# Kernel tuning notes

Hardware: AMD Instinct MI355X
Metric: run time of the kernel (lower is better)

## Reference

```python
import jax, jax.numpy as jnp
import numpy as np

B, D, L, E, R = 16384, 2048, 3, 8, 64


def setup_inputs() -> dict:
    key = jax.random.key(0)
    k1, k2, k3, k4 = jax.random.split(key, 4)
    scale = 1.0 / np.sqrt(D)  # ~ PyTorch Linear default init scale
    X0 = jax.random.normal(k1, (B, D), dtype=jnp.float32)
    U = jax.random.normal(k2, (L, E, R, D), dtype=jnp.float32) * scale
    V = jax.random.normal(k3, (L, E, R, D), dtype=jnp.float32) * scale
    Wg = jax.random.normal(k4, (L, E, D), dtype=jnp.float32) * scale
    bg = jnp.zeros((L, E), dtype=jnp.float32)
    return {"X0": X0, "U": U, "V": V, "Wg": Wg, "bg": bg}


def reference(X0, U, V, Wg, bg):
    # X0: (B, D); U, V: (L, E, R, D); Wg: (L, E, D); bg: (L, E)
    Xi = X0
    num_layers = U.shape[0]
    for l in range(num_layers):  # small fixed layer count
        gate = jax.nn.softmax(jnp.einsum('bd,ed->be', Xi, Wg[l]) + bg[l], axis=1)  # (B, E)
        Uo = jnp.einsum('bd,erd->ber', Xi, U[l])  # (B, E, R)
        Vo = jnp.einsum('bd,erd->ber', Xi, V[l])  # (B, E, R)
        expert_out = jnp.sum(Uo * Vo, axis=2)     # (B, E) low-rank bilinear forms
        xw = jnp.sum(expert_out * gate, axis=1, keepdims=True)  # (B, 1)
        Xi = Xi + X0 * xw  # residual cross update (dropout=0, eval mode)
    return Xi
```

## Files before the change

### kernel.cpp

```cpp
#include <hip/hip_runtime.h>
#include <hip/hip_bf16.h>

#define BDIM 16384
#define DDIM 2048
#define LNUM 3
#define ENUM 8
#define NP 24

#define BM 256
#define BK 64
#define NKIT (DDIM / BK)

typedef _Float16 f16x8 __attribute__((ext_vector_type(8)));
typedef _Float16 f16x4 __attribute__((ext_vector_type(4)));
typedef float f32x16 __attribute__((ext_vector_type(16)));


__global__ void cvt_w_kernel(const float* __restrict__ U, const float* __restrict__ V,
                             _Float16* __restrict__ Whf) {
    int idx = blockIdx.x * 256 + threadIdx.x;
    int f8     = idx & 255;
    int row128 = (idx >> 8) & 127;
    int p      = idx >> 15;
    const float* src = (row128 < 64)
        ? (U + ((size_t)(p * 64 + row128) * DDIM + f8 * 8))
        : (V + ((size_t)(p * 64 + (row128 - 64)) * DDIM + f8 * 8));
    float4 a = ((const float4*)src)[0];
    float4 b = ((const float4*)src)[1];
    f16x8 h = { (_Float16)a.x, (_Float16)a.y, (_Float16)a.z, (_Float16)a.w,
                (_Float16)b.x, (_Float16)b.y, (_Float16)b.z, (_Float16)b.w };
    int gn = row128 >> 5, col = row128 & 31;
    int kw = f8 >> 1, khalf = f8 & 1;
    size_t C = ((size_t)((p * 4 + gn) * 128 + kw)) * 64 + khalf * 32 + col;
    ((f16x8*)Whf)[C] = h;
}

__global__ __launch_bounds__(256, 2) void gate_kernel(
    const float* __restrict__ X0, const float* __restrict__ Wg,
    float* __restrict__ G, _Float16* __restrict__ X0f) {
    __shared__ float Wgs[NP * 256];
    const int tid = (int)threadIdx.x;
    const int rq  = tid >> 3;
    const int q   = tid & 7;
    const int r0  = blockIdx.x * 32 + rq;
    const int g32 = blockIdx.x;

    float acc[NP];
#pragma unroll
    for (int j = 0; j < NP; ++j) acc[j] = 0.f;

    const float4* xp = (const float4*)(X0 + (size_t)r0 * DDIM);

    for (int k0 = 0; k0 < DDIM; k0 += 256) {
        __syncthreads();
#pragma unroll
        for (int t = tid; t < NP * 64; t += 256)
            ((float4*)Wgs)[t] =
                ((const float4*)Wg)[(size_t)(t >> 6) * (DDIM / 4) + (k0 >> 2) + (t & 63)];
        __syncthreads();
#pragma unroll 2
        for (int i = 0; i < 4; ++i) {
            int f8 = i * 8 + q;
            int gcf4 = (k0 >> 2) + f8 * 2;
            float4 xa = xp[gcf4];
            float4 xb = xp[gcf4 + 1];
            f16x8 h = { (_Float16)xa.x, (_Float16)xa.y, (_Float16)xa.z, (_Float16)xa.w,
                        (_Float16)xb.x, (_Float16)xb.y, (_Float16)xb.z, (_Float16)xb.w };
            int kw = (k0 >> 4) + (f8 >> 1);
            int khalf = f8 & 1;
            ((f16x8*)X0f)[((size_t)(g32 * 128 + kw)) * 64 + khalf * 32 + rq] = h;
#pragma unroll
            for (int j = 0; j < NP; ++j) {
                float4 wa = ((const float4*)(Wgs + j * 256))[f8 * 2];
                float4 wb = ((const float4*)(Wgs + j * 256))[f8 * 2 + 1];
                acc[j] += xa.x * wa.x + xa.y * wa.y + xa.z * wa.z + xa.w * wa.w
                        + xb.x * wb.x + xb.y * wb.y + xb.z * wb.z + xb.w * wb.w;
            }
        }
    }
#pragma unroll
    for (int j = 0; j < NP; ++j) {
        float v = acc[j];
        v += __shfl_xor(v, 1);
        v += __shfl_xor(v, 2);
        v += __shfl_xor(v, 4);
        if (q == 0) G[(size_t)j * BDIM + r0] = v;
    }
}

__global__ __launch_bounds__(256, 2) void gemm_t_kernel(
    const _Float16* __restrict__ X0f,
    const _Float16* __restrict__ Whf,
    float* __restrict__ T)
{
    const int p    = blockIdx.y;
    const int m0   = blockIdx.x * BM;
    const int tid  = (int)threadIdx.x;
    const int wave = tid >> 6;
    const int lane = tid & 63;

    __shared__ _Float16 Bs[2 * 16 * 512];

    const int g32b = (m0 >> 5) + wave * 2;

    f32x16 acc[2][4];
#pragma unroll
    for (int i = 0; i < 2; ++i)
#pragma unroll
        for (int j = 0; j < 4; ++j) acc[i][j] = (f32x16)(0.f);

    f16x8 aF[2][8];

#pragma unroll
    for (int kw = 0; kw < 4; ++kw) {
        const _Float16* gb = Whf + (((size_t)((p * 4 + wave) * 128 + kw)) * 64 + lane) * 8;
        __builtin_amdgcn_global_load_lds(
            (const __attribute__((address_space(1))) void*)gb,
            (__attribute__((address_space(3))) void*)&Bs[(wave * 4 + kw) * 512], 16, 0, 0);
    }
#pragma unroll
    for (int mt = 0; mt < 2; ++mt)
#pragma unroll
        for (int kw = 0; kw < 4; ++kw)
            aF[0][mt * 4 + kw] = *(const f16x8*)(
                X0f + (((size_t)((g32b + mt) * 128 + kw)) * 64 + lane) * 8);
    __syncthreads();

#pragma unroll 2
    for (int it = 0; it < NKIT; ++it) {
        const int cur = it & 1, nxt = cur ^ 1;
        if (it != NKIT - 1) {
            const int kwn = (it + 1) * 4;
#pragma unroll
            for (int kw = 0; kw < 4; ++kw) {
                const _Float16* gb =
                    Whf + (((size_t)((p * 4 + wave) * 128 + kwn + kw)) * 64 + lane) * 8;
                __builtin_amdgcn_global_load_lds(
                    (const __attribute__((address_space(1))) void*)gb,
                    (__attribute__((address_space(3))) void*)&Bs[(nxt * 16 + wave * 4 + kw) * 512],
                    16, 0, 0);
            }
#pragma unroll
            for (int mt = 0; mt < 2; ++mt)
#pragma unroll
                for (int kw = 0; kw < 4; ++kw)
                    aF[nxt][mt * 4 + kw] = *(const f16x8*)(
                        X0f + (((size_t)((g32b + mt) * 128 + kwn + kw)) * 64 + lane) * 8);
        }
#pragma unroll
        for (int kw = 0; kw < 4; ++kw) {
            f16x8 bF[4];
#pragma unroll
            for (int gn = 0; gn < 4; ++gn)
                bF[gn] = *(const f16x8*)&Bs[((cur * 16 + gn * 4 + kw) * 64 + lane) * 8];
#pragma unroll
            for (int mt = 0; mt < 2; ++mt)
#pragma unroll
                for (int gn = 0; gn < 4; ++gn)
                    acc[mt][gn] = __builtin_amdgcn_mfma_f32_32x32x16_f16(
                        aF[cur][mt * 4 + kw], bF[gn], acc[mt][gn], 0, 0, 0);
        }
        __syncthreads();
    }

#pragma unroll
    for (int mt = 0; mt < 2; ++mt) {
#pragma unroll
        for (int reg = 0; reg < 16; ++reg) {
            float tp = acc[mt][0][reg] * acc[mt][2][reg]
                     + acc[mt][1][reg] * acc[mt][3][reg];
            tp += __shfl_xor(tp, 1);
            tp += __shfl_xor(tp, 2);
            tp += __shfl_xor(tp, 4);
            tp += __shfl_xor(tp, 8);
            tp += __shfl_xor(tp, 16);
            if ((lane & 31) == 0) {
                int row = (reg & 3) + 8 * (reg >> 2) + 4 * (lane >> 5);
                T[(size_t)p * BDIM + m0 + wave * 64 + mt * 32 + row] = tp;
            }
        }
    }
}

__global__ void epilogue_kernel(const _Float16* __restrict__ X0f,
                                const float* __restrict__ T,
                                const float* __restrict__ G,
                                const float* __restrict__ bg,
                                float* __restrict__ out) {
    __shared__ float s_sh[16];
    const int b0 = blockIdx.x * 16;
    const int tid = (int)threadIdx.x;
    if (tid < 16) {
        int b = b0 + tid;
        float s = 1.f;
#pragma unroll
        for (int l = 0; l < LNUM; ++l) {
            float logit[ENUM];
            float mx = -1e30f;
#pragma unroll
            for (int e = 0; e < ENUM; ++e) {
                int j = l * ENUM + e;
                float g = s * G[(size_t)j * BDIM + b] + bg[j];
                logit[e] = g;
                mx = fmaxf(mx, g);
            }
            float den = 0.f, num = 0.f;
            float s2 = s * s;
#pragma unroll
            for (int e = 0; e < ENUM; ++e) {
                int j = l * ENUM + e;
                float w = __expf(logit[e] - mx);
                den += w;
                num += w * (s2 * T[(size_t)j * BDIM + b]);
            }
            s += num / den;
        }
        s_sh[tid] = s;
    }
    __syncthreads();
    for (int idx = tid; idx < 16 * 256; idx += 256) {
        int r = idx >> 8;
        int c = idx & 255;
        int rg = b0 + r;
        float s = s_sh[r];
        f16x8 h = ((const f16x8*)X0f)[((size_t)((rg >> 5) * 128 + (c >> 1))) * 64
                                      + (c & 1) * 32 + (rg & 31)];
        float4 o0 = { s * (float)h[0], s * (float)h[1], s * (float)h[2], s * (float)h[3] };
        float4 o1 = { s * (float)h[4], s * (float)h[5], s * (float)h[6], s * (float)h[7] };
        float4* op = (float4*)(out + (size_t)rg * DDIM + c * 8);
        op[0] = o0;
        op[1] = o1;
    }
}

extern "C" void kernel_launch(void* const* d_in, const int* in_sizes, int n_in,
                              void* d_out, int out_size, void* d_ws, size_t ws_size,
                              hipStream_t stream) {
    const float* X0 = (const float*)d_in[0];
    const float* U  = (const float*)d_in[1];
    const float* V  = (const float*)d_in[2];
    const float* Wg = (const float*)d_in[3];
    const float* bg = (const float*)d_in[4];
    float* out = (float*)d_out;

    char* ws = (char*)d_ws;
    _Float16* X0f = (_Float16*)ws;
    _Float16* Whf = (_Float16*)(ws + 67108864ull);
    float* T      = (float*)(ws + 67108864ull + 12582912ull);
    float* G      = (float*)(ws + 67108864ull + 12582912ull + 1572864ull);

    cvt_w_kernel<<<dim3(NP * 128 * 256 / 256), dim3(256), 0, stream>>>(U, V, Whf);
    gate_kernel<<<dim3(BDIM / 32), dim3(256), 0, stream>>>(X0, Wg, G, X0f);
    gemm_t_kernel<<<dim3(BDIM / BM, NP), dim3(256), 0, stream>>>(X0f, Whf, T);
    epilogue_kernel<<<dim3(BDIM / 16), dim3(256), 0, stream>>>(X0f, T, G, bg, out);
}
```

Measured before the change: 549.7 us.

## Fuse weight conversion into gate kernel and epilogue into GEMM via counters

Merges the weight fp16 conversion into the gate kernel as extra blocks, and has gate blocks process two 32-row groups each. The GEMM doubles its K step per iteration and reorganises A-fragment prefetching. The last block to finish each 32-row group (tracked with atomic counters) computes the scalar recurrence and writes the output from fp32 X0. This removes two launches and the separate epilogue pass. It adds a memset and atomics, plus a tail where finishing blocks carry the epilogue, and the larger LDS buffer may reduce occupancy.

```diff
diff --git a/kernel.cpp b/kernel.cpp
--- a/kernel.cpp
+++ b/kernel.cpp
@@ -7,49 +7,51 @@
 #define ENUM 8
 #define NP 24
 
-#define BM 256
-#define BK 64
-#define NKIT (DDIM / BK)
+#define NKIT 16
 
 typedef _Float16 f16x8 __attribute__((ext_vector_type(8)));
 typedef _Float16 f16x4 __attribute__((ext_vector_type(4)));
 typedef float f32x16 __attribute__((ext_vector_type(16)));
 
 
-__global__ void cvt_w_kernel(const float* __restrict__ U, const float* __restrict__ V,
-                             _Float16* __restrict__ Whf) {
-    int idx = blockIdx.x * 256 + threadIdx.x;
-    int f8     = idx & 255;
-    int row128 = (idx >> 8) & 127;
-    int p      = idx >> 15;
-    const float* src = (row128 < 64)
-        ? (U + ((size_t)(p * 64 + row128) * DDIM + f8 * 8))
-        : (V + ((size_t)(p * 64 + (row128 - 64)) * DDIM + f8 * 8));
-    float4 a = ((const float4*)src)[0];
-    float4 b = ((const float4*)src)[1];
-    f16x8 h = { (_Float16)a.x, (_Float16)a.y, (_Float16)a.z, (_Float16)a.w,
-                (_Float16)b.x, (_Float16)b.y, (_Float16)b.z, (_Float16)b.w };
-    int gn = row128 >> 5, col = row128 & 31;
-    int kw = f8 >> 1, khalf = f8 & 1;
-    size_t C = ((size_t)((p * 4 + gn) * 128 + kw)) * 64 + khalf * 32 + col;
-    ((f16x8*)Whf)[C] = h;
-}
-
-__global__ __launch_bounds__(256, 2) void gate_kernel(
-    const float* __restrict__ X0, const float* __restrict__ Wg,
-    float* __restrict__ G, _Float16* __restrict__ X0f) {
+#define GATE_BLOCKS 256
+__global__ __launch_bounds__(256, 4) void prep_kernel(
+    const float* __restrict__ X0, const float* __restrict__ U,
+    const float* __restrict__ V, const float* __restrict__ Wg,
+    float* __restrict__ G, _Float16* __restrict__ X0f, _Float16* __restrict__ Whf) {
+    const int tid = (int)threadIdx.x;
+    if (blockIdx.x >= GATE_BLOCKS) {
+        int cidx = (blockIdx.x - GATE_BLOCKS) * 256 + tid;
+        int col   = cidx & 31;
+        int khalf = (cidx >> 5) & 1;
+        int kw    = (cidx >> 6) & 127;
+        int gn    = (cidx >> 13) & 3;
+        int p     = cidx >> 15;
+        int row128 = gn * 32 + col;
+        const float* src = (row128 < 64)
+            ? (U + ((size_t)(p * 64 + row128) * DDIM + kw * 16 + khalf * 8))
+            : (V + ((size_t)(p * 64 + (row128 - 64)) * DDIM + kw * 16 + khalf * 8));
+        float4 a = ((const float4*)src)[0];
+        float4 b = ((const float4*)src)[1];
+        f16x8 h = { (_Float16)a.x, (_Float16)a.y, (_Float16)a.z, (_Float16)a.w,
+                    (_Float16)b.x, (_Float16)b.y, (_Float16)b.z, (_Float16)b.w };
+        ((f16x8*)Whf)[cidx] = h;
+        return;
+    }
     __shared__ float Wgs[NP * 256];
-    const int tid = (int)threadIdx.x;
-    const int rq  = tid >> 3;
-    const int q   = tid & 7;
-    const int r0  = blockIdx.x * 32 + rq;
-    const int g32 = blockIdx.x;
-
-    float acc[NP];
-#pragma unroll
-    for (int j = 0; j < NP; ++j) acc[j] = 0.f;
-
-    const float4* xp = (const float4*)(X0 + (size_t)r0 * DDIM);
+    const int rq = tid >> 3;
+    const int q  = tid & 7;
+    const int r0 = blockIdx.x * 64 + rq;
+    const int g32a = blockIdx.x * 2, g32b_ = g32a + 1;
+
+    float acc[2][NP];
+#pragma unroll
+    for (int r = 0; r < 2; ++r)
+#pragma unroll
+        for (int j = 0; j < NP; ++j) acc[r][j] = 0.f;
+
+    const float4* x0p = (const float4*)(X0 + (size_t)r0 * DDIM);
+    const float4* x1p = (const float4*)(X0 + (size_t)(r0 + 32) * DDIM);
 
     for (int k0 = 0; k0 < DDIM; k0 += 256) {
         __syncthreads();
@@ -60,48 +62,66 @@
         __syncthreads();
 #pragma unroll 2
         for (int i = 0; i < 4; ++i) {
-            int f8 = i * 8 + q;
-            int gcf4 = (k0 >> 2) + f8 * 2;
-            float4 xa = xp[gcf4];
-            float4 xb = xp[gcf4 + 1];
-            f16x8 h = { (_Float16)xa.x, (_Float16)xa.y, (_Float16)xa.z, (_Float16)xa.w,
-                        (_Float16)xb.x, (_Float16)xb.y, (_Float16)xb.z, (_Float16)xb.w };
-            int kw = (k0 >> 4) + (f8 >> 1);
-            int khalf = f8 & 1;
-            ((f16x8*)X0f)[((size_t)(g32 * 128 + kw)) * 64 + khalf * 32 + rq] = h;
+            int f8l = i * 8 + q;
+            int gf4 = (k0 >> 2) + f8l * 2;
+            float4 xa = x0p[gf4], xb = x0p[gf4 + 1];
+            float4 ya = x1p[gf4], yb = x1p[gf4 + 1];
+            int f8g = (k0 >> 3) + f8l;
+            int kw = f8g >> 1, khalf = f8g & 1;
+            f16x8 h0 = { (_Float16)xa.x, (_Float16)xa.y, (_Float16)xa.z, (_Float16)xa.w,
+                         (_Float16)xb.x, (_Float16)xb.y, (_Float16)xb.z, (_Float16)xb.w };
+            f16x8 h1 = { (_Float16)ya.x, (_Float16)ya.y, (_Float16)ya.z, (_Float16)ya.w,
+                         (_Float16)yb.x, (_Float16)yb.y, (_Float16)yb.z, (_Float16)yb.w };
+            ((f16x8*)X0f)[((size_t)(g32a * 128 + kw)) * 64 + khalf * 32 + rq] = h0;
+            ((f16x8*)X0f)[((size_t)(g32b_ * 128 + kw)) * 64 + khalf * 32 + rq] = h1;
 #pragma unroll
             for (int j = 0; j < NP; ++j) {
-                float4 wa = ((const float4*)(Wgs + j * 256))[f8 * 2];
-                float4 wb = ((const float4*)(Wgs + j * 256))[f8 * 2 + 1];
-                acc[j] += xa.x * wa.x + xa.y * wa.y + xa.z * wa.z + xa.w * wa.w
-                        + xb.x * wb.x + xb.y * wb.y + xb.z * wb.z + xb.w * wb.w;
+                float4 wa = ((const float4*)(Wgs + j * 256))[f8l * 2];
+                float4 wb = ((const float4*)(Wgs + j * 256))[f8l * 2 + 1];
+                acc[0][j] += xa.x * wa.x + xa.y * wa.y + xa.z * wa.z + xa.w * wa.w
+                           + xb.x * wb.x + xb.y * wb.y + xb.z * wb.z + xb.w * wb.w;
+                acc[1][j] += ya.x * wa.x + ya.y * wa.y + ya.z * wa.z + ya.w * wa.w
+                           + yb.x * wb.x + yb.y * wb.y + yb.z * wb.z + yb.w * wb.w;
             }
         }
     }
 #pragma unroll
-    for (int j = 0; j < NP; ++j) {
-        float v = acc[j];
-        v += __shfl_xor(v, 1);
-        v += __shfl_xor(v, 2);
-        v += __shfl_xor(v, 4);
-        if (q == 0) G[(size_t)j * BDIM + r0] = v;
-    }
+    for (int r = 0; r < 2; ++r)
+#pragma unroll
+        for (int j = 0; j < NP; ++j) {
+            float v = acc[r][j];
+            v += __shfl_xor(v, 1);
+            v += __shfl_xor(v, 2);
+            v += __shfl_xor(v, 4);
+            if (q == 0) G[(size_t)j * BDIM + r0 + r * 32] = v;
+        }
 }
 
-__global__ __launch_bounds__(256, 2) void gemm_t_kernel(
+__global__ __launch_bounds__(256, 2) void gemm_epi_kernel(
     const _Float16* __restrict__ X0f,
     const _Float16* __restrict__ Whf,
-    float* __restrict__ T)
+    const float* __restrict__ X0,
+    const float* __restrict__ G,
+    const float* __restrict__ bg,
+    float* __restrict__ T,
+    unsigned int* __restrict__ cnt,
+    float* __restrict__ out)
 {
-    const int p    = blockIdx.y;
-    const int m0   = blockIdx.x * BM;
+    const int bx   = (int)blockIdx.x;
+    const int p    = bx % NP;
+    const int xb   = bx / NP;
+    const int m0   = xb * 256;
     const int tid  = (int)threadIdx.x;
     const int wave = tid >> 6;
     const int lane = tid & 63;
 
-    __shared__ _Float16 Bs[2 * 16 * 512];
-
-    const int g32b = (m0 >> 5) + wave * 2;
+    __shared__ _Float16 Bs[2 * 32 * 512];
+    __shared__ float s_sh[32];
+    __shared__ unsigned int won_sh;
+    if (tid == 0) won_sh = 0u;
+
+    const int g32b = xb * 8 + wave * 2;
+    const _Float16* Bp = Whf + ((size_t)(p * 4 + wave) * 128) * 512;
 
     f32x16 acc[2][4];
 #pragma unroll
@@ -112,53 +132,70 @@
     f16x8 aF[2][8];
 
 #pragma unroll
-    for (int kw = 0; kw < 4; ++kw) {
-        const _Float16* gb = Whf + (((size_t)((p * 4 + wave) * 128 + kw)) * 64 + lane) * 8;
+    for (int kw = 0; kw < 8; ++kw)
         __builtin_amdgcn_global_load_lds(
-            (const __attribute__((address_space(1))) void*)gb,
-            (__attribute__((address_space(3))) void*)&Bs[(wave * 4 + kw) * 512], 16, 0, 0);
-    }
+            (const __attribute__((address_space(1))) void*)(Bp + (size_t)kw * 512 + lane * 8),
+            (__attribute__((address_space(3))) void*)&Bs[(wave * 8 + kw) * 512], 16, 0, 0);
 #pragma unroll
     for (int mt = 0; mt < 2; ++mt)
 #pragma unroll
-        for (int kw = 0; kw < 4; ++kw)
-            aF[0][mt * 4 + kw] = *(const f16x8*)(
-                X0f + (((size_t)((g32b + mt) * 128 + kw)) * 64 + lane) * 8);
+        for (int i = 0; i < 4; ++i)
+            aF[0][mt * 4 + i] = *(const f16x8*)(
+                X0f + ((size_t)((g32b + mt) * 128 + i)) * 512 + lane * 8);
     __syncthreads();
 
-#pragma unroll 2
+#pragma unroll 1
     for (int it = 0; it < NKIT; ++it) {
         const int cur = it & 1, nxt = cur ^ 1;
+        const int kb = it * 8;
         if (it != NKIT - 1) {
-            const int kwn = (it + 1) * 4;
-#pragma unroll
-            for (int kw = 0; kw < 4; ++kw) {
-                const _Float16* gb =
-                    Whf + (((size_t)((p * 4 + wave) * 128 + kwn + kw)) * 64 + lane) * 8;
+#pragma unroll
+            for (int kw = 0; kw < 8; ++kw)
                 __builtin_amdgcn_global_load_lds(
-                    (const __attribute__((address_space(1))) void*)gb,
-                    (__attribute__((address_space(3))) void*)&Bs[(nxt * 16 + wave * 4 + kw) * 512],
+                    (const __attribute__((address_space(1))) void*)(
+                        Bp + (size_t)(kb + 8 + kw) * 512 + lane * 8),
+                    (__attribute__((address_space(3))) void*)&Bs[(nxt * 32 + wave * 8 + kw) * 512],
                     16, 0, 0);
-            }
-#pragma unroll
-            for (int mt = 0; mt < 2; ++mt)
-#pragma unroll
-                for (int kw = 0; kw < 4; ++kw)
-                    aF[nxt][mt * 4 + kw] = *(const f16x8*)(
-                        X0f + (((size_t)((g32b + mt) * 128 + kwn + kw)) * 64 + lane) * 8);
-        }
-#pragma unroll
-        for (int kw = 0; kw < 4; ++kw) {
+        }
+#pragma unroll
+        for (int mt = 0; mt < 2; ++mt)
+#pragma unroll
+            for (int i = 0; i < 4; ++i)
+                aF[1][mt * 4 + i] = *(const f16x8*)(
+                    X0f + ((size_t)((g32b + mt) * 128 + kb + 4 + i)) * 512 + lane * 8);
+#pragma unroll
+        for (int i = 0; i < 4; ++i) {
             f16x8 bF[4];
 #pragma unroll
             for (int gn = 0; gn < 4; ++gn)
-                bF[gn] = *(const f16x8*)&Bs[((cur * 16 + gn * 4 + kw) * 64 + lane) * 8];
+                bF[gn] = *(const f16x8*)&Bs[(cur * 32 + gn * 8 + i) * 512 + lane * 8];
 #pragma unroll
             for (int mt = 0; mt < 2; ++mt)
 #pragma unroll
                 for (int gn = 0; gn < 4; ++gn)
                     acc[mt][gn] = __builtin_amdgcn_mfma_f32_32x32x16_f16(
-                        aF[cur][mt * 4 + kw], bF[gn], acc[mt][gn], 0, 0, 0);
+                        aF[0][mt * 4 + i], bF[gn], acc[mt][gn], 0, 0, 0);
+        }
+        if (it != NKIT - 1) {
+#pragma unroll
+            for (int mt = 0; mt < 2; ++mt)
+#pragma unroll
+                for (int i = 0; i < 4; ++i)
+                    aF[0][mt * 4 + i] = *(const f16x8*)(
+                        X0f + ((size_t)((g32b + mt) * 128 + kb + 8 + i)) * 512 + lane * 8);
+        }
+#pragma unroll
+        for (int i = 0; i < 4; ++i) {
+            f16x8 bF[4];
+#pragma unroll
+            for (int gn = 0; gn < 4; ++gn)
+                bF[gn] = *(const f16x8*)&Bs[(cur * 32 + gn * 8 + 4 + i) * 512 + lane * 8];
+#pragma unroll
+            for (int mt = 0; mt < 2; ++mt)
+#pragma unroll
+                for (int gn = 0; gn < 4; ++gn)
+                    acc[mt][gn] = __builtin_amdgcn_mfma_f32_32x32x16_f16(
+                        aF[1][mt * 4 + i], bF[gn], acc[mt][gn], 0, 0, 0);
         }
         __syncthreads();
     }
@@ -180,56 +217,57 @@
             }
         }
     }
-}
-
-__global__ void epilogue_kernel(const _Float16* __restrict__ X0f,
-                                const float* __restrict__ T,
-                                const float* __restrict__ G,
-                                const float* __restrict__ bg,
-                                float* __restrict__ out) {
-    __shared__ float s_sh[16];
-    const int b0 = blockIdx.x * 16;
-    const int tid = (int)threadIdx.x;
-    if (tid < 16) {
-        int b = b0 + tid;
-        float s = 1.f;
-#pragma unroll
-        for (int l = 0; l < LNUM; ++l) {
-            float logit[ENUM];
-            float mx = -1e30f;
-#pragma unroll
-            for (int e = 0; e < ENUM; ++e) {
-                int j = l * ENUM + e;
-                float g = s * G[(size_t)j * BDIM + b] + bg[j];
-                logit[e] = g;
-                mx = fmaxf(mx, g);
+
+    __threadfence();
+    __syncthreads();
+    if (tid < 8) {
+        unsigned old = atomicAdd(&cnt[xb * 8 + tid], 1u);
+        if (old == NP - 1) atomicOr(&won_sh, 1u << tid);
+    }
+    __syncthreads();
+    unsigned won = won_sh;
+    if (won) __threadfence();
+    while (won) {
+        int qg = __ffs(won) - 1;
+        won &= won - 1u;
+        int r0 = m0 + qg * 32;
+        if (tid < 32) {
+            int b = r0 + tid;
+            float s = 1.f;
+#pragma unroll
+            for (int l = 0; l < LNUM; ++l) {
+                float logit[ENUM];
+                float mx = -1e30f;
+#pragma unroll
+                for (int e = 0; e < ENUM; ++e) {
+                    int j = l * ENUM + e;
+                    float g = s * G[(size_t)j * BDIM + b] + bg[j];
+                    logit[e] = g;
+                    mx = fmaxf(mx, g);
+                }
+                float den = 0.f, num = 0.f;
+                float s2 = s * s;
+#pragma unroll
+                for (int e = 0; e < ENUM; ++e) {
+                    int j = l * ENUM + e;
+                    float w = __expf(logit[e] - mx);
+                    den += w;
+                    num += w * (s2 * T[(size_t)j * BDIM + b]);
+                }
+                s += num / den;
             }
-            float den = 0.f, num = 0.f;
-            float s2 = s * s;
-#pragma unroll
-            for (int e = 0; e < ENUM; ++e) {
-                int j = l * ENUM + e;
-                float w = __expf(logit[e] - mx);
-                den += w;
-                num += w * (s2 * T[(size_t)j * BDIM + b]);
-            }
-            s += num / den;
-        }
-        s_sh[tid] = s;
-    }
-    __syncthreads();
-    for (int idx = tid; idx < 16 * 256; idx += 256) {
-        int r = idx >> 8;
-        int c = idx & 255;
-        int rg = b0 + r;
-        float s = s_sh[r];
-        f16x8 h = ((const f16x8*)X0f)[((size_t)((rg >> 5) * 128 + (c >> 1))) * 64
-                                      + (c & 1) * 32 + (rg & 31)];
-        float4 o0 = { s * (float)h[0], s * (float)h[1], s * (float)h[2], s * (float)h[3] };
-        float4 o1 = { s * (float)h[4], s * (float)h[5], s * (float)h[6], s * (float)h[7] };
-        float4* op = (float4*)(out + (size_t)rg * DDIM + c * 8);
-        op[0] = o0;
-        op[1] = o1;
+            s_sh[tid] = s;
+        }
+        __syncthreads();
+        for (int idx = tid; idx < 32 * 512; idx += 256) {
+            int r = idx >> 9;
+            int c = idx & 511;
+            float s = s_sh[r];
+            float4 x = ((const float4*)(X0 + (size_t)(r0 + r) * DDIM))[c];
+            x.x *= s; x.y *= s; x.z *= s; x.w *= s;
+            ((float4*)(out + (size_t)(r0 + r) * DDIM))[c] = x;
+        }
+        __syncthreads();
     }
 }
 
@@ -248,9 +286,11 @@
     _Float16* Whf = (_Float16*)(ws + 67108864ull);
     float* T      = (float*)(ws + 67108864ull + 12582912ull);
     float* G      = (float*)(ws + 67108864ull + 12582912ull + 1572864ull);
-
-    cvt_w_kernel<<<dim3(NP * 128 * 256 / 256), dim3(256), 0, stream>>>(U, V, Whf);
-    gate_kernel<<<dim3(BDIM / 32), dim3(256), 0, stream>>>(X0, Wg, G, X0f);
-    gemm_t_kernel<<<dim3(BDIM / BM, NP), dim3(256), 0, stream>>>(X0f, Whf, T);
-    epilogue_kernel<<<dim3(BDIM / 16), dim3(256), 0, stream>>>(X0f, T, G, bg, out);
+    unsigned int* cnt = (unsigned int*)(ws + 67108864ull + 12582912ull + 2 * 1572864ull);
+
+    hipMemsetAsync((void*)cnt, 0, (BDIM / 32) * sizeof(unsigned int), stream);
+    prep_kernel<<<dim3(GATE_BLOCKS + NP * 128 * 256 / 256), dim3(256), 0, stream>>>(
+        X0, U, V, Wg, G, X0f, Whf);
+    gemm_epi_kernel<<<dim3((BDIM / 256) * NP), dim3(256), 0, stream>>>(
+        X0f, Whf, X0, G, bg, T, cnt, out);
 }
```

Result: slower. 1.263 ms (+129.8%).
